# Optimization experiments

Measured on AMD Instinct MI355X. Metric: run time of the kernel, lower is better.

Reference implementation:

```python
import jax, jax.numpy as jnp
import numpy as np

B, T, C = 16, 64, 512


def setup_inputs() -> dict:
    key = jax.random.key(0)
    ks = jax.random.split(key, 12)
    s = 1.0 / np.sqrt(C)
    st = 1.0 / np.sqrt(2.0)
    return {
        "x": jax.random.normal(ks[0], (B, T, C), dtype=jnp.float32),
        "ts": jax.random.uniform(ks[1], (B, T), dtype=jnp.float32),
        "attn_mask": jnp.ones((B, T), dtype=jnp.float32),
        # project: Linear(C, C)
        "W_proj": jax.random.uniform(ks[2], (C, C), jnp.float32, -s, s),
        "b_proj": jax.random.uniform(ks[3], (C,), jnp.float32, -s, s),
        # embed_xs: Linear(C, C)
        "W_x": jax.random.uniform(ks[4], (C, C), jnp.float32, -s, s),
        "b_x": jax.random.uniform(ks[5], (C,), jnp.float32, -s, s),
        # embed_ts: Linear(2, C)
        "W_t": jax.random.uniform(ks[6], (2, C), jnp.float32, -st, st),
        "b_t": jax.random.uniform(ks[7], (C,), jnp.float32, -st, st),
        # get_importances Linear(C, C)
        "W_imp": jax.random.uniform(ks[8], (C, C), jnp.float32, -s, s),
        "b_imp": jax.random.uniform(ks[9], (C,), jnp.float32, -s, s),
    }


def reference(x, ts, attn_mask, W_proj, b_proj, W_x, b_x, W_t, b_t, W_imp, b_imp):
    # x: [B,T,C], ts: [B,T], attn_mask: [B,T]
    values = (x @ W_proj + b_proj)[:, None, :, :]          # [B,1,T,C]
    rel = ts[:, :, None] - ts[:, None, :]                  # [B,T,T]
    rel2 = jnp.log1p(jnp.maximum(jnp.stack([rel, -rel], axis=-1), 0.0))  # [B,T,T,2]
    h = rel2 @ W_t + b_t                                   # [B,T,T,C] (include_t)
    h = h + (x @ W_x + b_x)[:, None, :, :]                 # include_x, broadcast over dim 1
    importances = jax.nn.sigmoid(jax.nn.relu(h) @ W_imp + b_imp)  # [B,T,T,C]
    importances = importances * attn_mask[:, None, :, None]
    interactions = jax.nn.logsumexp(values * importances, axis=2)  # [B,T,C]
    return (x + interactions, importances.mean(axis=3))
```

## Files before the change

kernel.cpp:

```cpp
#include <hip/hip_runtime.h>

#define Bn 16
#define Tn 64
#define Cn 512
#define LDA 520

typedef short s8v __attribute__((ext_vector_type(8)));
typedef float f4v __attribute__((ext_vector_type(4)));

__device__ __forceinline__ unsigned short f2bf(float f){
  union { float f; unsigned int u; } c; c.f = f;
  return (unsigned short)((c.u + 0x7FFFu + ((c.u >> 16) & 1u)) >> 16);
}
__device__ __forceinline__ float bf2f(unsigned short u){
  union { unsigned int u; float f; } c; c.u = ((unsigned int)u) << 16; return c.f;
}

__global__ void swz(const float* __restrict__ Wp, const float* __restrict__ Wx,
                    const float* __restrict__ Wi, unsigned short* __restrict__ dstall){
  int gid = blockIdx.x * 256 + threadIdx.x;
  int mat = gid >> 15;
  int rem = gid & 32767;
  int lane = rem & 63;
  int st   = rem >> 6;
  int t    = st & 31;
  int s    = st >> 5;
  int n  = t * 16 + (lane & 15);
  int k0 = s * 32 + ((lane >> 4) << 3);
  const float* W = (mat == 0) ? Wp : ((mat == 1) ? Wx : Wi);
  unsigned int p[4];
#pragma unroll
  for(int q = 0; q < 4; ++q){
    unsigned short lo = f2bf(W[(k0 + 2*q    ) * Cn + n]);
    unsigned short hi = f2bf(W[(k0 + 2*q + 1) * Cn + n]);
    p[q] = (unsigned int)lo | ((unsigned int)hi << 16);
  }
  uint4 o; o.x = p[0]; o.y = p[1]; o.z = p[2]; o.w = p[3];
  *reinterpret_cast<uint4*>(dstall + (size_t)mat * 262144 + (size_t)rem * 8) = o;
}

__global__ void prep(const float* __restrict__ x, const float* __restrict__ bp,
                     const float* __restrict__ bx, const unsigned short* __restrict__ WswP,
                     const unsigned short* __restrict__ WswX,
                     float* __restrict__ xe, unsigned short* __restrict__ vbf){
  __shared__ unsigned short lA[Tn * LDA];
  const int b = blockIdx.x >> 1, mat = blockIdx.x & 1;
  const int tid = threadIdx.x;
  const int c0 = (tid & 127) * 4, jb = tid >> 7;
#pragma unroll
  for(int it = 0; it < 16; ++it){
    int j = jb + it * 4;
    f4v xv = *reinterpret_cast<const f4v*>(x + ((b * Tn + j) * Cn + c0));
    uint2 uu;
    uu.x = (unsigned int)f2bf(xv[0]) | ((unsigned int)f2bf(xv[1]) << 16);
    uu.y = (unsigned int)f2bf(xv[2]) | ((unsigned int)f2bf(xv[3]) << 16);
    *reinterpret_cast<uint2*>(&lA[j * LDA + c0]) = uu;
  }
  __syncthreads();
  const unsigned short* Wsw = mat ? WswX : WswP;
  const float* bias = mat ? bx : bp;
  const int lane = tid & 63, w = tid >> 6, quad = lane >> 4, ln = lane & 15;
  f4v acc[4][4];
#pragma unroll
  for(int mt = 0; mt < 4; ++mt)
#pragma unroll
    for(int nt = 0; nt < 4; ++nt){
      acc[mt][nt][0] = 0.f; acc[mt][nt][1] = 0.f; acc[mt][nt][2] = 0.f; acc[mt][nt][3] = 0.f;
    }
#pragma unroll 1
  for(int s = 0; s < 16; ++s){
    s8v af[4], bfv[4];
#pragma unroll
    for(int mt = 0; mt < 4; ++mt)
      af[mt] = *reinterpret_cast<const s8v*>(&lA[(mt * 16 + ln) * LDA + s * 32 + quad * 8]);
#pragma unroll
    for(int nt = 0; nt < 4; ++nt)
      bfv[nt] = *reinterpret_cast<const s8v*>(Wsw + (((s * 32) + (w * 4 + nt)) * 64 + lane) * 8);
#pragma unroll
    for(int mt = 0; mt < 4; ++mt)
#pragma unroll
      for(int nt = 0; nt < 4; ++nt)
        acc[mt][nt] = __builtin_amdgcn_mfma_f32_16x16x32_bf16(af[mt], bfv[nt], acc[mt][nt], 0, 0, 0);
  }
#pragma unroll
  for(int nt = 0; nt < 4; ++nt){
    int c = w * 64 + nt * 16 + ln;
    float bb = bias[c];
#pragma unroll
    for(int mt = 0; mt < 4; ++mt)
#pragma unroll
      for(int r = 0; r < 4; ++r){
        int j = mt * 16 + quad * 4 + r;
        float v = acc[mt][nt][r] + bb;
        int idx = (b * Tn + j) * Cn + c;
        if(mat == 0) vbf[idx] = f2bf(v);
        else         xe[idx]  = v;
      }
  }
}

__global__ void fused(const float* __restrict__ x, const float* __restrict__ ts,
                      const float* __restrict__ am, const float* __restrict__ Wt,
                      const float* __restrict__ bt, const float* __restrict__ bimp,
                      const unsigned short* __restrict__ Wsw,
                      const float* __restrict__ xe, const unsigned short* __restrict__ vbf,
                      float* __restrict__ out0, float* __restrict__ out1){
  __shared__ unsigned short lA[Tn * LDA];
  __shared__ float tss[Tn], msk[Tn], rsum[Tn];
  const int b = blockIdx.x >> 6, i = blockIdx.x & 63;
  const int tid = threadIdx.x;
  if(tid < Tn){ tss[tid] = ts[b * Tn + tid]; msk[tid] = am[b * Tn + tid]; rsum[tid] = 0.f; }
  __syncthreads();
  const int c0 = (tid & 127) * 4, jb = tid >> 7;
  const float tsi = tss[i];
  f4v wt0 = *reinterpret_cast<const f4v*>(Wt + c0);
  f4v wt1 = *reinterpret_cast<const f4v*>(Wt + Cn + c0);
  f4v btv = *reinterpret_cast<const f4v*>(bt + c0);
#pragma unroll
  for(int it = 0; it < 16; ++it){
    int j = jb + it * 4;
    float d  = tsi - tss[j];
    float r0 = __logf(1.f + fmaxf(d, 0.f));
    float r1 = __logf(1.f + fmaxf(-d, 0.f));
    f4v xv = *reinterpret_cast<const f4v*>(xe + ((b * Tn + j) * Cn + c0));
    float h0 = fmaxf(xv[0] + r0 * wt0[0] + r1 * wt1[0] + btv[0], 0.f);
    float h1 = fmaxf(xv[1] + r0 * wt0[1] + r1 * wt1[1] + btv[1], 0.f);
    float h2 = fmaxf(xv[2] + r0 * wt0[2] + r1 * wt1[2] + btv[2], 0.f);
    float h3 = fmaxf(xv[3] + r0 * wt0[3] + r1 * wt1[3] + btv[3], 0.f);
    uint2 uu;
    uu.x = (unsigned int)f2bf(h0) | ((unsigned int)f2bf(h1) << 16);
    uu.y = (unsigned int)f2bf(h2) | ((unsigned int)f2bf(h3) << 16);
    *reinterpret_cast<uint2*>(&lA[j * LDA + c0]) = uu;
  }
  __syncthreads();

  const int lane = tid & 63, w = tid >> 6, quad = lane >> 4, ln = lane & 15;
  f4v acc[4][4];
#pragma unroll
  for(int mt = 0; mt < 4; ++mt)
#pragma unroll
    for(int nt = 0; nt < 4; ++nt){
      acc[mt][nt][0] = 0.f; acc[mt][nt][1] = 0.f; acc[mt][nt][2] = 0.f; acc[mt][nt][3] = 0.f;
    }
#pragma unroll 1
  for(int s = 0; s < 16; ++s){
    s8v af[4], bfv[4];
#pragma unroll
    for(int mt = 0; mt < 4; ++mt)
      af[mt] = *reinterpret_cast<const s8v*>(&lA[(mt * 16 + ln) * LDA + s * 32 + quad * 8]);
#pragma unroll
    for(int nt = 0; nt < 4; ++nt)
      bfv[nt] = *reinterpret_cast<const s8v*>(Wsw + (((s * 32) + (w * 4 + nt)) * 64 + lane) * 8);
#pragma unroll
    for(int mt = 0; mt < 4; ++mt)
#pragma unroll
      for(int nt = 0; nt < 4; ++nt)
        acc[mt][nt] = __builtin_amdgcn_mfma_f32_16x16x32_bf16(af[mt], bfv[nt], acc[mt][nt], 0, 0, 0);
  }

#pragma unroll
  for(int nt = 0; nt < 4; ++nt){
    int c = w * 64 + nt * 16 + ln;
    float bb = bimp[c];
#pragma unroll
    for(int mt = 0; mt < 4; ++mt)
#pragma unroll
      for(int r = 0; r < 4; ++r){
        int j = mt * 16 + quad * 4 + r;
        float z = acc[mt][nt][r] + bb;
        float im = msk[j] * __builtin_amdgcn_rcpf(1.f + __expf(-z));
        acc[mt][nt][r] = im;
      }
  }

#pragma unroll
  for(int mt = 0; mt < 4; ++mt)
#pragma unroll
    for(int r = 0; r < 4; ++r){
      float p = acc[mt][0][r] + acc[mt][1][r] + acc[mt][2][r] + acc[mt][3][r];
      p += __shfl_xor(p, 1, 64);
      p += __shfl_xor(p, 2, 64);
      p += __shfl_xor(p, 4, 64);
      p += __shfl_xor(p, 8, 64);
      if(ln == 0) atomicAdd(&rsum[mt * 16 + quad * 4 + r], p);
    }
  __syncthreads();

#pragma unroll
  for(int it = 0; it < 16; ++it){
    int j = jb + it * 4;
    *reinterpret_cast<uint2*>(&lA[j * LDA + c0]) =
        *reinterpret_cast<const uint2*>(vbf + (b * Tn + j) * Cn + c0);
  }
  __syncthreads();

#pragma unroll
  for(int nt = 0; nt < 4; ++nt){
    int c = w * 64 + nt * 16 + ln;
    float se = 0.f;
#pragma unroll
    for(int mt = 0; mt < 4; ++mt)
#pragma unroll
      for(int r = 0; r < 4; ++r){
        float v = bf2f(lA[(mt * 16 + quad * 4 + r) * LDA + c]);
        se += __expf(v * acc[mt][nt][r]);
      }
    se += __shfl_xor(se, 16, 64);
    se += __shfl_xor(se, 32, 64);
    if(quad == 0){
      int idx = (b * Tn + i) * Cn + c;
      out0[idx] = x[idx] + __logf(se);
    }
  }
  if(tid < Tn) out1[(b * Tn + i) * Tn + tid] = rsum[tid] * (1.f / 512.f);
}

extern "C" void kernel_launch(void* const* d_in, const int* in_sizes, int n_in,
                              void* d_out, int out_size, void* d_ws, size_t ws_size,
                              hipStream_t stream){
  const float* x    = (const float*)d_in[0];
  const float* ts   = (const float*)d_in[1];
  const float* am   = (const float*)d_in[2];
  const float* Wp   = (const float*)d_in[3];
  const float* bp   = (const float*)d_in[4];
  const float* Wx   = (const float*)d_in[5];
  const float* bx   = (const float*)d_in[6];
  const float* Wt   = (const float*)d_in[7];
  const float* bt   = (const float*)d_in[8];
  const float* Wi   = (const float*)d_in[9];
  const float* bimp = (const float*)d_in[10];
  float* out0 = (float*)d_out;
  float* out1 = out0 + Bn * Tn * Cn;

  char* ws = (char*)d_ws;
  unsigned short* Wsw = (unsigned short*)ws;
  float* xe = (float*)(ws + 3 * 524288);
  unsigned short* vbf = (unsigned short*)(ws + 3 * 524288 + 2097152);

  swz<<<384, 256, 0, stream>>>(Wp, Wx, Wi, Wsw);
  prep<<<32, 512, 0, stream>>>(x, bp, bx, Wsw, Wsw + 262144, xe, vbf);
  fused<<<1024, 512, 0, stream>>>(x, ts, am, Wt, bt, bimp, Wsw + 2 * 262144,
                                  xe, vbf, out0, out1);
}
```

Baseline: 148.1 us.

## Precompute log-time features, store values in MFMA fragment layout, use exp2/log2

The log1p time features are now computed once in the swizzle kernel instead of in every fused block. The projected values are pre-scaled by log2(e) and written straight into the per-wave MFMA accumulator fragment layout, so the fused kernel loads them into registers and skips the LDS staging pass and one barrier. The embed_ts bias is folded into xe. The sigmoid and logsumexp now use exp2/log2 intrinsics, and prep is split over twice as many blocks. The cost is an extra workspace buffer and bf16 rounding of the scaled values.

```diff
diff --git a/kernel.cpp b/kernel.cpp
--- a/kernel.cpp
+++ b/kernel.cpp
@@ -1,10 +1,14 @@
 #include <hip/hip_runtime.h>
+#include <hip/hip_bf16.h>
 
 #define Bn 16
 #define Tn 64
 #define Cn 512
 #define LDA 520
 
+#define LOG2E 1.4426950408889634f
+#define LN2   0.6931471805599453f
+
 typedef short s8v __attribute__((ext_vector_type(8)));
 typedef float f4v __attribute__((ext_vector_type(4)));
 
@@ -12,54 +16,72 @@
   union { float f; unsigned int u; } c; c.f = f;
   return (unsigned short)((c.u + 0x7FFFu + ((c.u >> 16) & 1u)) >> 16);
 }
-__device__ __forceinline__ float bf2f(unsigned short u){
-  union { unsigned int u; float f; } c; c.u = ((unsigned int)u) << 16; return c.f;
+__device__ __forceinline__ unsigned int pk2bf(float a, float b){
+  __hip_bfloat162 t = __float22bfloat162_rn(make_float2(a, b));
+  union { __hip_bfloat162 h; unsigned int u; } c; c.h = t; return c.u;
+}
+__device__ __forceinline__ float bits2f(unsigned int u){
+  union { unsigned int u; float f; } c; c.u = u; return c.f;
 }
 
 __global__ void swz(const float* __restrict__ Wp, const float* __restrict__ Wx,
-                    const float* __restrict__ Wi, unsigned short* __restrict__ dstall){
-  int gid = blockIdx.x * 256 + threadIdx.x;
-  int mat = gid >> 15;
-  int rem = gid & 32767;
-  int lane = rem & 63;
-  int st   = rem >> 6;
-  int t    = st & 31;
-  int s    = st >> 5;
-  int n  = t * 16 + (lane & 15);
-  int k0 = s * 32 + ((lane >> 4) << 3);
-  const float* W = (mat == 0) ? Wp : ((mat == 1) ? Wx : Wi);
-  unsigned int p[4];
-#pragma unroll
-  for(int q = 0; q < 4; ++q){
-    unsigned short lo = f2bf(W[(k0 + 2*q    ) * Cn + n]);
-    unsigned short hi = f2bf(W[(k0 + 2*q + 1) * Cn + n]);
-    p[q] = (unsigned int)lo | ((unsigned int)hi << 16);
-  }
-  uint4 o; o.x = p[0]; o.y = p[1]; o.z = p[2]; o.w = p[3];
-  *reinterpret_cast<uint4*>(dstall + (size_t)mat * 262144 + (size_t)rem * 8) = o;
-}
-
-__global__ void prep(const float* __restrict__ x, const float* __restrict__ bp,
-                     const float* __restrict__ bx, const unsigned short* __restrict__ WswP,
-                     const unsigned short* __restrict__ WswX,
-                     float* __restrict__ xe, unsigned short* __restrict__ vbf){
+                    const float* __restrict__ Wi, const float* __restrict__ ts,
+                    unsigned short* __restrict__ dstall, float* __restrict__ R){
+  if(blockIdx.x < 384){
+    int gid = blockIdx.x * 256 + threadIdx.x;
+    int mat = gid >> 15;
+    int rem = gid & 32767;
+    int lane = rem & 63;
+    int st   = rem >> 6;
+    int t    = st & 31;
+    int s    = st >> 5;
+    int n  = t * 16 + (lane & 15);
+    int k0 = s * 32 + ((lane >> 4) << 3);
+    const float* W = (mat == 0) ? Wp : ((mat == 1) ? Wx : Wi);
+    unsigned int p[4];
+#pragma unroll
+    for(int q = 0; q < 4; ++q)
+      p[q] = pk2bf(W[(k0 + 2*q) * Cn + n], W[(k0 + 2*q + 1) * Cn + n]);
+    uint4 o; o.x = p[0]; o.y = p[1]; o.z = p[2]; o.w = p[3];
+    *reinterpret_cast<uint4*>(dstall + (size_t)mat * 262144 + (size_t)rem * 8) = o;
+  } else {
+    int gid2 = (blockIdx.x - 384) * 256 + threadIdx.x;
+    float r[8];
+#pragma unroll
+    for(int q = 0; q < 4; ++q){
+      int p = gid2 * 4 + q;
+      int b = p >> 12, i = (p >> 6) & 63, j = p & 63;
+      float d = ts[b * Tn + i] - ts[b * Tn + j];
+      r[2*q]   = __logf(1.f + fmaxf(d, 0.f));
+      r[2*q+1] = __logf(1.f + fmaxf(-d, 0.f));
+    }
+    float4* Rf4 = reinterpret_cast<float4*>(R);
+    Rf4[gid2 * 2    ] = make_float4(r[0], r[1], r[2], r[3]);
+    Rf4[gid2 * 2 + 1] = make_float4(r[4], r[5], r[6], r[7]);
+  }
+}
+
+__global__ __launch_bounds__(256, 4)
+void prep(const float* __restrict__ x, const float* __restrict__ bp,
+          const float* __restrict__ bx, const float* __restrict__ bt,
+          const unsigned short* __restrict__ WswP,
+          const unsigned short* __restrict__ WswX,
+          float* __restrict__ xe, unsigned short* __restrict__ vfrag){
   __shared__ unsigned short lA[Tn * LDA];
-  const int b = blockIdx.x >> 1, mat = blockIdx.x & 1;
+  const int b = blockIdx.x >> 2, mat = (blockIdx.x >> 1) & 1, half = blockIdx.x & 1;
   const int tid = threadIdx.x;
   const int c0 = (tid & 127) * 4, jb = tid >> 7;
 #pragma unroll
-  for(int it = 0; it < 16; ++it){
-    int j = jb + it * 4;
+  for(int it = 0; it < 32; ++it){
+    int j = jb + it * 2;
     f4v xv = *reinterpret_cast<const f4v*>(x + ((b * Tn + j) * Cn + c0));
-    uint2 uu;
-    uu.x = (unsigned int)f2bf(xv[0]) | ((unsigned int)f2bf(xv[1]) << 16);
-    uu.y = (unsigned int)f2bf(xv[2]) | ((unsigned int)f2bf(xv[3]) << 16);
+    uint2 uu; uu.x = pk2bf(xv[0], xv[1]); uu.y = pk2bf(xv[2], xv[3]);
     *reinterpret_cast<uint2*>(&lA[j * LDA + c0]) = uu;
   }
   __syncthreads();
   const unsigned short* Wsw = mat ? WswX : WswP;
-  const float* bias = mat ? bx : bp;
-  const int lane = tid & 63, w = tid >> 6, quad = lane >> 4, ln = lane & 15;
+  const int lane = tid & 63, w2 = tid >> 6, quad = lane >> 4, ln = lane & 15;
+  const int wg = half * 4 + w2;
   f4v acc[4][4];
 #pragma unroll
   for(int mt = 0; mt < 4; ++mt)
@@ -75,61 +97,78 @@
       af[mt] = *reinterpret_cast<const s8v*>(&lA[(mt * 16 + ln) * LDA + s * 32 + quad * 8]);
 #pragma unroll
     for(int nt = 0; nt < 4; ++nt)
-      bfv[nt] = *reinterpret_cast<const s8v*>(Wsw + (((s * 32) + (w * 4 + nt)) * 64 + lane) * 8);
+      bfv[nt] = *reinterpret_cast<const s8v*>(Wsw + (((s * 32) + (wg * 4 + nt)) * 64 + lane) * 8);
 #pragma unroll
     for(int mt = 0; mt < 4; ++mt)
 #pragma unroll
       for(int nt = 0; nt < 4; ++nt)
         acc[mt][nt] = __builtin_amdgcn_mfma_f32_16x16x32_bf16(af[mt], bfv[nt], acc[mt][nt], 0, 0, 0);
   }
-#pragma unroll
-  for(int nt = 0; nt < 4; ++nt){
-    int c = w * 64 + nt * 16 + ln;
-    float bb = bias[c];
-#pragma unroll
-    for(int mt = 0; mt < 4; ++mt)
-#pragma unroll
-      for(int r = 0; r < 4; ++r){
-        int j = mt * 16 + quad * 4 + r;
-        float v = acc[mt][nt][r] + bb;
-        int idx = (b * Tn + j) * Cn + c;
-        if(mat == 0) vbf[idx] = f2bf(v);
-        else         xe[idx]  = v;
+  if(mat == 0){
+#pragma unroll
+    for(int eb = 0; eb < 8; ++eb){
+      int mt = eb >> 1, ntb = (eb & 1) * 2;
+      unsigned int wds[4];
+#pragma unroll
+      for(int h = 0; h < 2; ++h){
+        int nt = ntb + h;
+        float bb = bp[wg * 64 + nt * 16 + ln];
+        float v0 = (acc[mt][nt][0] + bb) * LOG2E;
+        float v1 = (acc[mt][nt][1] + bb) * LOG2E;
+        float v2 = (acc[mt][nt][2] + bb) * LOG2E;
+        float v3 = (acc[mt][nt][3] + bb) * LOG2E;
+        wds[h*2]   = pk2bf(v0, v1);
+        wds[h*2+1] = pk2bf(v2, v3);
       }
-  }
-}
-
-__global__ void fused(const float* __restrict__ x, const float* __restrict__ ts,
-                      const float* __restrict__ am, const float* __restrict__ Wt,
-                      const float* __restrict__ bt, const float* __restrict__ bimp,
-                      const unsigned short* __restrict__ Wsw,
-                      const float* __restrict__ xe, const unsigned short* __restrict__ vbf,
-                      float* __restrict__ out0, float* __restrict__ out1){
+      uint4 o; o.x = wds[0]; o.y = wds[1]; o.z = wds[2]; o.w = wds[3];
+      *reinterpret_cast<uint4*>(vfrag + ((size_t)((b * 8 + wg) * 8 + eb) * 64 + lane) * 8) = o;
+    }
+  } else {
+#pragma unroll
+    for(int nt = 0; nt < 4; ++nt){
+      int c = wg * 64 + nt * 16 + ln;
+      float bb = bx[c] + bt[c];
+#pragma unroll
+      for(int mt = 0; mt < 4; ++mt)
+#pragma unroll
+        for(int r = 0; r < 4; ++r){
+          int j = mt * 16 + quad * 4 + r;
+          xe[(b * Tn + j) * Cn + c] = acc[mt][nt][r] + bb;
+        }
+    }
+  }
+}
+
+__global__ __launch_bounds__(512, 4)
+void fused(const float* __restrict__ x, const float* __restrict__ am,
+           const float* __restrict__ Wt, const float* __restrict__ bimp,
+           const unsigned short* __restrict__ Wsw, const float* __restrict__ R,
+           const float* __restrict__ xe, const unsigned short* __restrict__ vfrag,
+           float* __restrict__ out0, float* __restrict__ out1){
   __shared__ unsigned short lA[Tn * LDA];
-  __shared__ float tss[Tn], msk[Tn], rsum[Tn];
+  __shared__ float msk[Tn], rr0[Tn], rr1[Tn], rsum[Tn];
   const int b = blockIdx.x >> 6, i = blockIdx.x & 63;
   const int tid = threadIdx.x;
-  if(tid < Tn){ tss[tid] = ts[b * Tn + tid]; msk[tid] = am[b * Tn + tid]; rsum[tid] = 0.f; }
+  if(tid < Tn){
+    msk[tid] = am[b * Tn + tid];
+    rsum[tid] = 0.f;
+    float2 rv = reinterpret_cast<const float2*>(R)[(b * Tn + i) * Tn + tid];
+    rr0[tid] = rv.x; rr1[tid] = rv.y;
+  }
   __syncthreads();
   const int c0 = (tid & 127) * 4, jb = tid >> 7;
-  const float tsi = tss[i];
   f4v wt0 = *reinterpret_cast<const f4v*>(Wt + c0);
   f4v wt1 = *reinterpret_cast<const f4v*>(Wt + Cn + c0);
-  f4v btv = *reinterpret_cast<const f4v*>(bt + c0);
 #pragma unroll
   for(int it = 0; it < 16; ++it){
     int j = jb + it * 4;
-    float d  = tsi - tss[j];
-    float r0 = __logf(1.f + fmaxf(d, 0.f));
-    float r1 = __logf(1.f + fmaxf(-d, 0.f));
+    float r0 = rr0[j], r1 = rr1[j];
     f4v xv = *reinterpret_cast<const f4v*>(xe + ((b * Tn + j) * Cn + c0));
-    float h0 = fmaxf(xv[0] + r0 * wt0[0] + r1 * wt1[0] + btv[0], 0.f);
-    float h1 = fmaxf(xv[1] + r0 * wt0[1] + r1 * wt1[1] + btv[1], 0.f);
-    float h2 = fmaxf(xv[2] + r0 * wt0[2] + r1 * wt1[2] + btv[2], 0.f);
-    float h3 = fmaxf(xv[3] + r0 * wt0[3] + r1 * wt1[3] + btv[3], 0.f);
-    uint2 uu;
-    uu.x = (unsigned int)f2bf(h0) | ((unsigned int)f2bf(h1) << 16);
-    uu.y = (unsigned int)f2bf(h2) | ((unsigned int)f2bf(h3) << 16);
+    float h0 = fmaxf(fmaf(r1, wt1[0], fmaf(r0, wt0[0], xv[0])), 0.f);
+    float h1 = fmaxf(fmaf(r1, wt1[1], fmaf(r0, wt0[1], xv[1])), 0.f);
+    float h2 = fmaxf(fmaf(r1, wt1[2], fmaf(r0, wt0[2], xv[2])), 0.f);
+    float h3 = fmaxf(fmaf(r1, wt1[3], fmaf(r0, wt0[3], xv[3])), 0.f);
+    uint2 uu; uu.x = pk2bf(h0, h1); uu.y = pk2bf(h2, h3);
     *reinterpret_cast<uint2*>(&lA[j * LDA + c0]) = uu;
   }
   __syncthreads();
@@ -158,26 +197,27 @@
         acc[mt][nt] = __builtin_amdgcn_mfma_f32_16x16x32_bf16(af[mt], bfv[nt], acc[mt][nt], 0, 0, 0);
   }
 
-#pragma unroll
-  for(int nt = 0; nt < 4; ++nt){
-    int c = w * 64 + nt * 16 + ln;
-    float bb = bimp[c];
-#pragma unroll
-    for(int mt = 0; mt < 4; ++mt)
-#pragma unroll
-      for(int r = 0; r < 4; ++r){
-        int j = mt * 16 + quad * 4 + r;
-        float z = acc[mt][nt][r] + bb;
-        float im = msk[j] * __builtin_amdgcn_rcpf(1.f + __expf(-z));
+  uint4 vv[8];
+#pragma unroll
+  for(int eb = 0; eb < 8; ++eb)
+    vv[eb] = *reinterpret_cast<const uint4*>(vfrag + ((size_t)((b * 8 + w) * 8 + eb) * 64 + lane) * 8);
+
+  float bb[4];
+#pragma unroll
+  for(int nt = 0; nt < 4; ++nt) bb[nt] = bimp[w * 64 + nt * 16 + ln];
+#pragma unroll
+  for(int mt = 0; mt < 4; ++mt)
+#pragma unroll
+    for(int r = 0; r < 4; ++r){
+      float mk = msk[mt * 16 + quad * 4 + r];
+      float p = 0.f;
+#pragma unroll
+      for(int nt = 0; nt < 4; ++nt){
+        float z = acc[mt][nt][r] + bb[nt];
+        float im = mk * __builtin_amdgcn_rcpf(1.f + __builtin_amdgcn_exp2f(z * -LOG2E));
         acc[mt][nt][r] = im;
+        p += im;
       }
-  }
-
-#pragma unroll
-  for(int mt = 0; mt < 4; ++mt)
-#pragma unroll
-    for(int r = 0; r < 4; ++r){
-      float p = acc[mt][0][r] + acc[mt][1][r] + acc[mt][2][r] + acc[mt][3][r];
       p += __shfl_xor(p, 1, 64);
       p += __shfl_xor(p, 2, 64);
       p += __shfl_xor(p, 4, 64);
@@ -185,34 +225,28 @@
       if(ln == 0) atomicAdd(&rsum[mt * 16 + quad * 4 + r], p);
     }
   __syncthreads();
-
-#pragma unroll
-  for(int it = 0; it < 16; ++it){
-    int j = jb + it * 4;
-    *reinterpret_cast<uint2*>(&lA[j * LDA + c0]) =
-        *reinterpret_cast<const uint2*>(vbf + (b * Tn + j) * Cn + c0);
-  }
-  __syncthreads();
-
+  if(tid < Tn) out1[(b * Tn + i) * Tn + tid] = rsum[tid] * (1.f / 512.f);
+
+  const unsigned int* vw = reinterpret_cast<const unsigned int*>(vv);
 #pragma unroll
   for(int nt = 0; nt < 4; ++nt){
-    int c = w * 64 + nt * 16 + ln;
     float se = 0.f;
 #pragma unroll
     for(int mt = 0; mt < 4; ++mt)
 #pragma unroll
       for(int r = 0; r < 4; ++r){
-        float v = bf2f(lA[(mt * 16 + quad * 4 + r) * LDA + c]);
-        se += __expf(v * acc[mt][nt][r]);
+        int e = mt * 16 + nt * 4 + r;
+        unsigned int d = vw[e >> 1];
+        float vl = bits2f((e & 1) ? (d & 0xffff0000u) : (d << 16));
+        se += __builtin_amdgcn_exp2f(vl * acc[mt][nt][r]);
       }
     se += __shfl_xor(se, 16, 64);
     se += __shfl_xor(se, 32, 64);
     if(quad == 0){
-      int idx = (b * Tn + i) * Cn + c;
-      out0[idx] = x[idx] + __logf(se);
-    }
-  }
-  if(tid < Tn) out1[(b * Tn + i) * Tn + tid] = rsum[tid] * (1.f / 512.f);
+      int idx = (b * Tn + i) * Cn + (w * 64 + nt * 16 + ln);
+      out0[idx] = x[idx] + __builtin_amdgcn_logf(se) * LN2;
+    }
+  }
 }
 
 extern "C" void kernel_launch(void* const* d_in, const int* in_sizes, int n_in,
@@ -233,12 +267,13 @@
   float* out1 = out0 + Bn * Tn * Cn;
 
   char* ws = (char*)d_ws;
-  unsigned short* Wsw = (unsigned short*)ws;
-  float* xe = (float*)(ws + 3 * 524288);
-  unsigned short* vbf = (unsigned short*)(ws + 3 * 524288 + 2097152);
-
-  swz<<<384, 256, 0, stream>>>(Wp, Wx, Wi, Wsw);
-  prep<<<32, 512, 0, stream>>>(x, bp, bx, Wsw, Wsw + 262144, xe, vbf);
-  fused<<<1024, 512, 0, stream>>>(x, ts, am, Wt, bt, bimp, Wsw + 2 * 262144,
-                                  xe, vbf, out0, out1);
-}
+  unsigned short* Wsw   = (unsigned short*)ws;
+  float*          xe    = (float*)(ws + 3 * 524288);
+  unsigned short* vfrag = (unsigned short*)(ws + 3*524288 + 2097152);
+  float*          R     = (float*)(ws + 3*524288 + 2097152 + 1048576);
+
+  swz<<<448, 256, 0, stream>>>(Wp, Wx, Wi, ts, Wsw, R);
+  prep<<<64, 256, 0, stream>>>(x, bp, bx, bt, Wsw, Wsw + 262144, xe, vfrag);
+  fused<<<1024, 512, 0, stream>>>(x, am, Wt, bimp, Wsw + 2 * 262144, R,
+                                  xe, vfrag, out0, out1);
+}
```

Result: faster. 135.1 us (-8.7%).
